# Kernel optimization log

Hardware: AMD Instinct MI355X
Metric: run time of the kernel (lower is better)

Reference implementation:

```python
import jax, jax.numpy as jnp
import numpy as np

B, C, T, H, W = 8, 64, 32, 56, 56
WIN = 7
EPS = 1e-5


def setup_inputs() -> dict:
    key = jax.random.key(0)
    k1, k2, k3, k4 = jax.random.split(key, 4)
    x = jax.random.normal(k1, (B, C, T, H, W), dtype=jnp.float32)
    # BatchNorm3d affine params (randomized slightly around init for nontrivial math)
    gamma = 1.0 + 0.1 * jax.random.normal(k2, (C,), dtype=jnp.float32)
    beta = 0.1 * jax.random.normal(k3, (C,), dtype=jnp.float32)
    # rpconv1d weight [2] ~ init [1,0] plus noise so both taps contribute
    rpw = jnp.array([1.0, 0.0], dtype=jnp.float32) + 0.1 * jax.random.normal(k4, (2,), dtype=jnp.float32)
    return {"x": x, "gamma": gamma, "beta": beta, "rpw": rpw, "w": WIN}


def reference(x, gamma, beta, rpw, w):
    # x: [B, C, T, H, W]
    Bs, Cs, Ts, Hs, Ws = x.shape
    # rank-pooling weights: for window position k (0-based), 2*(k+1) - w - 1
    coeff = (2.0 * jnp.arange(1, w + 1, dtype=x.dtype) - w - 1)
    # causal padding with w-1 zero frames at the front of T
    xp = jnp.pad(x, ((0, 0), (0, 0), (w - 1, 0), (0, 0), (0, 0)))
    rp = jnp.zeros_like(x)
    for k in range(w):  # small fixed window, fuses under XLA
        rp = rp + coeff[k] * jax.lax.dynamic_slice_in_dim(xp, k, Ts, axis=2)
    # BatchNorm3d (training-mode batch stats over B,T,H,W per channel) + ReLU
    mean = jnp.mean(rp, axis=(0, 2, 3, 4), keepdims=True)
    var = jnp.var(rp, axis=(0, 2, 3, 4), keepdims=True)
    bn = (rp - mean) * jax.lax.rsqrt(var + EPS)
    bn = bn * gamma.reshape(1, -1, 1, 1, 1) + beta.reshape(1, -1, 1, 1, 1)
    y = jax.nn.relu(bn)
    # gating: (y + 1) * x
    g = (y + 1.0) * x
    # rpconv1d(2->1, kernel 1, no bias): out = rpw[0]*x + rpw[1]*g
    return rpw[0] * x + rpw[1] * g
```

## Files before the change

kernel.cpp:

```cpp
#include <hip/hip_runtime.h>

#define B_      8
#define C_      64
#define T_      32
#define HW_     3136
#define HW4_    784
#define PLANE_  (T_ * HW_)
#define NPC_    802816.0
#define EPS_    1e-5
#define BLK_    512
#define TAIL_   (HW4_ - BLK_)

typedef float f32x4 __attribute__((ext_vector_type(4)));

__device__ __forceinline__ float rp_tap(float a0, float a1, float a2,
                                        float a4, float a5, float a6) {
    return 6.f * (a0 - a6) + 4.f * (a1 - a5) + 2.f * (a2 - a4);
}

__device__ __forceinline__ float rp_tap4_sq(const f32x4& a0, const f32x4& a1,
                                            const f32x4& a2, const f32x4& a4,
                                            const f32x4& a5, const f32x4& a6,
                                            float& s, float& q) {
#pragma unroll
    for (int j = 0; j < 4; ++j) {
        float r = rp_tap(a0[j], a1[j], a2[j], a4[j], a5[j], a6[j]);
        s += r;
        q += r * r;
    }
    return 0.f;
}

__global__ __launch_bounds__(BLK_, 2) void datt_pass1(
    const float* __restrict__ x, double2* __restrict__ part)
{
    const int bc  = blockIdx.x;
    const int tid = threadIdx.x;
    const bool act1 = tid < TAIL_;

    const f32x4* xp = (const f32x4*)(x + (size_t)bc * PLANE_);

    f32x4 w0[7], w1[7];
#pragma unroll
    for (int k = 0; k < 7; ++k) { w0[k] = (f32x4)(0.f); w1[k] = (f32x4)(0.f); }

    float s = 0.f, q = 0.f;
#pragma unroll
    for (int t = 0; t < T_; ++t) {
        const int row = t * HW4_;
        f32x4 x0 = xp[row + tid];
        f32x4 x1 = act1 ? xp[row + BLK_ + tid] : (f32x4)(0.f);
        w0[t % 7] = x0;
        w1[t % 7] = x1;
        rp_tap4_sq(x0, w0[(t + 6) % 7], w0[(t + 5) % 7],
                       w0[(t + 3) % 7], w0[(t + 2) % 7], w0[(t + 1) % 7], s, q);
        rp_tap4_sq(x1, w1[(t + 6) % 7], w1[(t + 5) % 7],
                       w1[(t + 3) % 7], w1[(t + 2) % 7], w1[(t + 1) % 7], s, q);
    }
#pragma unroll
    for (int off = 32; off; off >>= 1) {
        s += __shfl_down(s, off);
        q += __shfl_down(q, off);
    }
    __shared__ double ls[8], lq[8];
    const int wid  = tid >> 6;
    const int lane = tid & 63;
    if (lane == 0) { ls[wid] = (double)s; lq[wid] = (double)q; }
    __syncthreads();
    if (tid == 0) {
        double S = 0.0, Q = 0.0;
#pragma unroll
        for (int i = 0; i < 8; ++i) { S += ls[i]; Q += lq[i]; }
        part[bc] = make_double2(S, Q);
    }
}

__global__ __launch_bounds__(BLK_, 2) void datt_pass2(
    const float* __restrict__ x,
    const double2* __restrict__ part,
    const float* __restrict__ gamma,
    const float* __restrict__ beta,
    const float* __restrict__ rpw,
    float* __restrict__ out)
{
    const int bc  = blockIdx.x;
    const int c   = bc & (C_ - 1);
    const int tid = threadIdx.x;
    const bool act1 = tid < TAIL_;

    __shared__ float lss[2];

    if (tid < 64) {
        double s = 0.0, q = 0.0;
        if (tid < B_) {
            double2 p = part[tid * C_ + c];
            s = p.x; q = p.y;
        }
#pragma unroll
        for (int off = 4; off; off >>= 1) {
            s += __shfl_down(s, off);
            q += __shfl_down(q, off);
        }
        if (tid == 0) {
            double mean = s / NPC_;
            double var  = q / NPC_ - mean * mean;
            float rstd  = (float)(1.0 / sqrt(var + EPS_));
            float sc    = gamma[c] * rstd;
            lss[0] = sc;
            lss[1] = beta[c] - (float)mean * sc;
        }
    }
    __syncthreads();

    const float sc = lss[0];
    const float sh = lss[1];
    const float r1 = rpw[1];
    const float A  = rpw[0] + r1;

    const f32x4* xp = (const f32x4*)(x   + (size_t)bc * PLANE_);
    f32x4*       op = (f32x4*)      (out + (size_t)bc * PLANE_);

    f32x4 w0[7], w1[7];
#pragma unroll
    for (int k = 0; k < 7; ++k) { w0[k] = (f32x4)(0.f); w1[k] = (f32x4)(0.f); }

#pragma unroll
    for (int t = 0; t < T_; ++t) {
        const int row = t * HW4_;
        f32x4 x0 = xp[row + tid];
        f32x4 x1 = act1 ? xp[row + BLK_ + tid] : (f32x4)(0.f);
        w0[t % 7] = x0;
        w1[t % 7] = x1;

        f32x4 o0, o1;
        {
            const f32x4 a1 = w0[(t + 6) % 7], a2 = w0[(t + 5) % 7];
            const f32x4 a4 = w0[(t + 3) % 7], a5 = w0[(t + 2) % 7];
            const f32x4 a6 = w0[(t + 1) % 7];
#pragma unroll
            for (int j = 0; j < 4; ++j) {
                float yj = fmaxf(fmaf(rp_tap(x0[j], a1[j], a2[j], a4[j], a5[j], a6[j]),
                                      sc, sh), 0.f);
                o0[j] = x0[j] * fmaf(r1, yj, A);
            }
        }
        {
            const f32x4 a1 = w1[(t + 6) % 7], a2 = w1[(t + 5) % 7];
            const f32x4 a4 = w1[(t + 3) % 7], a5 = w1[(t + 2) % 7];
            const f32x4 a6 = w1[(t + 1) % 7];
#pragma unroll
            for (int j = 0; j < 4; ++j) {
                float yj = fmaxf(fmaf(rp_tap(x1[j], a1[j], a2[j], a4[j], a5[j], a6[j]),
                                      sc, sh), 0.f);
                o1[j] = x1[j] * fmaf(r1, yj, A);
            }
        }
        __builtin_nontemporal_store(o0, &op[row + tid]);
        if (act1)
            __builtin_nontemporal_store(o1, &op[row + BLK_ + tid]);
    }
}

extern "C" void kernel_launch(void* const* d_in, const int* in_sizes, int n_in,
                              void* d_out, int out_size, void* d_ws, size_t ws_size,
                              hipStream_t stream) {
    const float* x     = (const float*)d_in[0];
    const float* gamma = (const float*)d_in[1];
    const float* beta  = (const float*)d_in[2];
    const float* rpw   = (const float*)d_in[3];
    float* out = (float*)d_out;

    double2* part = (double2*)d_ws;

    datt_pass1<<<dim3(B_ * C_), BLK_, 0, stream>>>(x, part);
    datt_pass2<<<dim3(B_ * C_), BLK_, 0, stream>>>(x, part, gamma, beta, rpw, out);
}
```

Measured before the change: 384.0 us.

## Fuse stats and apply passes into one cooperative kernel with per-channel atomics

Merges the two passes into a single cooperative launch. Each block atomically adds its partial sums to per-channel accumulators, then spins until all 8 batch blocks of its channel have arrived before applying the normalization. The aim is to remove the second kernel launch and let the second read of the plane hit in cache while it is still warm. In exchange it adds a memset and system-scope atomics, and it depends on the cooperative launch succeeding, with a fallback to the old two-kernel path.

```diff
diff --git a/kernel.cpp b/kernel.cpp
--- a/kernel.cpp
+++ b/kernel.cpp
@@ -18,17 +18,139 @@
     return 6.f * (a0 - a6) + 4.f * (a1 - a5) + 2.f * (a2 - a4);
 }
 
-__device__ __forceinline__ float rp_tap4_sq(const f32x4& a0, const f32x4& a1,
-                                            const f32x4& a2, const f32x4& a4,
-                                            const f32x4& a5, const f32x4& a6,
-                                            float& s, float& q) {
-#pragma unroll
-    for (int j = 0; j < 4; ++j) {
-        float r = rp_tap(a0[j], a1[j], a2[j], a4[j], a5[j], a6[j]);
-        s += r;
-        q += r * r;
-    }
-    return 0.f;
+__global__ __launch_bounds__(BLK_, 4) void datt_fused(
+    const float* __restrict__ x,
+    const float* __restrict__ gamma,
+    const float* __restrict__ beta,
+    const float* __restrict__ rpw,
+    float* __restrict__ out,
+    double* chanS,
+    double* chanQ,
+    unsigned* ctr)
+{
+    const int bc  = blockIdx.x;
+    const int c   = bc & (C_ - 1);
+    const int tid = threadIdx.x;
+    const bool act1 = tid < TAIL_;
+
+    const f32x4* xp = (const f32x4*)(x + (size_t)bc * PLANE_);
+
+    f32x4 w0[7], w1[7];
+#pragma unroll
+    for (int k = 0; k < 7; ++k) { w0[k] = (f32x4)(0.f); w1[k] = (f32x4)(0.f); }
+
+    float s = 0.f, q = 0.f;
+#pragma unroll
+    for (int t = 0; t < T_; ++t) {
+        const int row = t * HW4_;
+        f32x4 x0 = xp[row + tid];
+        f32x4 x1 = act1 ? xp[row + BLK_ + tid] : (f32x4)(0.f);
+        w0[t % 7] = x0;
+        w1[t % 7] = x1;
+        {
+            const f32x4 a1 = w0[(t + 6) % 7], a2 = w0[(t + 5) % 7];
+            const f32x4 a4 = w0[(t + 3) % 7], a5 = w0[(t + 2) % 7];
+            const f32x4 a6 = w0[(t + 1) % 7];
+#pragma unroll
+            for (int j = 0; j < 4; ++j) {
+                float r = rp_tap(x0[j], a1[j], a2[j], a4[j], a5[j], a6[j]);
+                s += r; q += r * r;
+            }
+        }
+        {
+            const f32x4 a1 = w1[(t + 6) % 7], a2 = w1[(t + 5) % 7];
+            const f32x4 a4 = w1[(t + 3) % 7], a5 = w1[(t + 2) % 7];
+            const f32x4 a6 = w1[(t + 1) % 7];
+#pragma unroll
+            for (int j = 0; j < 4; ++j) {
+                float r = rp_tap(x1[j], a1[j], a2[j], a4[j], a5[j], a6[j]);
+                s += r; q += r * r;
+            }
+        }
+    }
+#pragma unroll
+    for (int off = 32; off; off >>= 1) {
+        s += __shfl_down(s, off);
+        q += __shfl_down(q, off);
+    }
+    __shared__ double ls[8], lq[8];
+    __shared__ float lss[2];
+    const int wid  = tid >> 6;
+    const int lane = tid & 63;
+    if (lane == 0) { ls[wid] = (double)s; lq[wid] = (double)q; }
+    __syncthreads();
+
+    if (tid == 0) {
+        double S = 0.0, Q = 0.0;
+#pragma unroll
+        for (int i = 0; i < 8; ++i) { S += ls[i]; Q += lq[i]; }
+        __hip_atomic_fetch_add(&chanS[c], S, __ATOMIC_SEQ_CST,
+                               __HIP_MEMORY_SCOPE_SYSTEM);
+        __hip_atomic_fetch_add(&chanQ[c], Q, __ATOMIC_SEQ_CST,
+                               __HIP_MEMORY_SCOPE_SYSTEM);
+        __hip_atomic_fetch_add(&ctr[c], 1u, __ATOMIC_SEQ_CST,
+                               __HIP_MEMORY_SCOPE_SYSTEM);
+        while (__hip_atomic_load(&ctr[c], __ATOMIC_SEQ_CST,
+                                 __HIP_MEMORY_SCOPE_SYSTEM) < (unsigned)B_)
+            __builtin_amdgcn_s_sleep(8);
+        double S8 = __hip_atomic_load(&chanS[c], __ATOMIC_SEQ_CST,
+                                      __HIP_MEMORY_SCOPE_SYSTEM);
+        double Q8 = __hip_atomic_load(&chanQ[c], __ATOMIC_SEQ_CST,
+                                      __HIP_MEMORY_SCOPE_SYSTEM);
+        double mean = S8 / NPC_;
+        double var  = Q8 / NPC_ - mean * mean;
+        float rstd  = (float)(1.0 / sqrt(var + EPS_));
+        float sc    = gamma[c] * rstd;
+        lss[0] = sc;
+        lss[1] = beta[c] - (float)mean * sc;
+    }
+    __syncthreads();
+
+    const float sc = lss[0];
+    const float sh = lss[1];
+    const float r1 = rpw[1];
+    const float A  = rpw[0] + r1;
+
+    f32x4* op = (f32x4*)(out + (size_t)bc * PLANE_);
+
+#pragma unroll
+    for (int k = 0; k < 7; ++k) { w0[k] = (f32x4)(0.f); w1[k] = (f32x4)(0.f); }
+
+#pragma unroll
+    for (int t = 0; t < T_; ++t) {
+        const int row = t * HW4_;
+        f32x4 x0 = xp[row + tid];
+        f32x4 x1 = act1 ? xp[row + BLK_ + tid] : (f32x4)(0.f);
+        w0[t % 7] = x0;
+        w1[t % 7] = x1;
+
+        f32x4 o0, o1;
+        {
+            const f32x4 a1 = w0[(t + 6) % 7], a2 = w0[(t + 5) % 7];
+            const f32x4 a4 = w0[(t + 3) % 7], a5 = w0[(t + 2) % 7];
+            const f32x4 a6 = w0[(t + 1) % 7];
+#pragma unroll
+            for (int j = 0; j < 4; ++j) {
+                float yj = fmaxf(fmaf(rp_tap(x0[j], a1[j], a2[j], a4[j], a5[j], a6[j]),
+                                      sc, sh), 0.f);
+                o0[j] = x0[j] * fmaf(r1, yj, A);
+            }
+        }
+        {
+            const f32x4 a1 = w1[(t + 6) % 7], a2 = w1[(t + 5) % 7];
+            const f32x4 a4 = w1[(t + 3) % 7], a5 = w1[(t + 2) % 7];
+            const f32x4 a6 = w1[(t + 1) % 7];
+#pragma unroll
+            for (int j = 0; j < 4; ++j) {
+                float yj = fmaxf(fmaf(rp_tap(x1[j], a1[j], a2[j], a4[j], a5[j], a6[j]),
+                                      sc, sh), 0.f);
+                o1[j] = x1[j] * fmaf(r1, yj, A);
+            }
+        }
+        __builtin_nontemporal_store(o0, &op[row + tid]);
+        if (act1)
+            __builtin_nontemporal_store(o1, &op[row + BLK_ + tid]);
+    }
 }
 
 __global__ __launch_bounds__(BLK_, 2) void datt_pass1(
@@ -52,10 +174,26 @@
         f32x4 x1 = act1 ? xp[row + BLK_ + tid] : (f32x4)(0.f);
         w0[t % 7] = x0;
         w1[t % 7] = x1;
-        rp_tap4_sq(x0, w0[(t + 6) % 7], w0[(t + 5) % 7],
-                       w0[(t + 3) % 7], w0[(t + 2) % 7], w0[(t + 1) % 7], s, q);
-        rp_tap4_sq(x1, w1[(t + 6) % 7], w1[(t + 5) % 7],
-                       w1[(t + 3) % 7], w1[(t + 2) % 7], w1[(t + 1) % 7], s, q);
+        {
+            const f32x4 a1 = w0[(t + 6) % 7], a2 = w0[(t + 5) % 7];
+            const f32x4 a4 = w0[(t + 3) % 7], a5 = w0[(t + 2) % 7];
+            const f32x4 a6 = w0[(t + 1) % 7];
+#pragma unroll
+            for (int j = 0; j < 4; ++j) {
+                float r = rp_tap(x0[j], a1[j], a2[j], a4[j], a5[j], a6[j]);
+                s += r; q += r * r;
+            }
+        }
+        {
+            const f32x4 a1 = w1[(t + 6) % 7], a2 = w1[(t + 5) % 7];
+            const f32x4 a4 = w1[(t + 3) % 7], a5 = w1[(t + 2) % 7];
+            const f32x4 a6 = w1[(t + 1) % 7];
+#pragma unroll
+            for (int j = 0; j < 4; ++j) {
+                float r = rp_tap(x1[j], a1[j], a2[j], a4[j], a5[j], a6[j]);
+                s += r; q += r * r;
+            }
+        }
     }
 #pragma unroll
     for (int off = 32; off; off >>= 1) {
@@ -170,8 +308,23 @@
     const float* rpw   = (const float*)d_in[3];
     float* out = (float*)d_out;
 
-    double2* part = (double2*)d_ws;
-
-    datt_pass1<<<dim3(B_ * C_), BLK_, 0, stream>>>(x, part);
-    datt_pass2<<<dim3(B_ * C_), BLK_, 0, stream>>>(x, part, gamma, beta, rpw, out);
-}
+    double*   chanS = (double*)d_ws;
+    double*   chanQ = chanS + C_;
+    unsigned* ctr   = (unsigned*)(chanQ + C_);
+
+    hipMemsetAsync(d_ws, 0, 2 * C_ * sizeof(double) + C_ * sizeof(unsigned),
+                   stream);
+
+    void* args[] = {(void*)&x, (void*)&gamma, (void*)&beta, (void*)&rpw,
+                    (void*)&out, (void*)&chanS, (void*)&chanQ, (void*)&ctr};
+    hipError_t e = hipLaunchCooperativeKernel((const void*)datt_fused,
+                                              dim3(B_ * C_), dim3(BLK_),
+                                              args, 0, stream);
+    if (e != hipSuccess) {
+        (void)hipGetLastError();
+        double2* part = (double2*)d_ws;
+        datt_pass1<<<dim3(B_ * C_), BLK_, 0, stream>>>(x, part);
+        datt_pass2<<<dim3(B_ * C_), BLK_, 0, stream>>>(x, part, gamma, beta,
+                                                       rpw, out);
+    }
+}
```

Result: slower. 543.5 us (+41.6%).
